# Kernel optimization log

Measured on AMD Instinct MI355X. Metric: run time of the kernel, lower is better.

## Reference

```python
import jax, jax.numpy as jnp
import numpy as np

N = 128          # preconditioner matrix dim = 8*8*2
L8 = 8           # lattice extent
KAPPA = 0.276
MAXITER = 20
NENT = N * (N + 1) // 2  # 8256 lower-triangular entries
_rows, _cols = np.tril_indices(N)

G = [jnp.array([[0, 1], [1, 0]], dtype=jnp.complex64),          # gamma_1 = sigma_x
     jnp.array([[0, -1j], [1j, 0]], dtype=jnp.complex64)]        # gamma_2 = sigma_y
I2 = jnp.eye(2, dtype=jnp.complex64)


def _D(x, U):
    # Wilson-Dirac: x (B,8,8,2) spinor field, U (B,2,8,8) complex links.
    out = x
    for mu in range(2):
        ax = mu + 1
        Um = U[:, mu]                                  # U_mu(n)
        Umb = jnp.roll(jnp.conj(Um), 1, axis=ax)       # U_mu^dag(n-mu)
        fwd = Um[..., None] * jnp.roll(x, -1, axis=ax)  # U(n) x(n+mu)
        bwd = Umb[..., None] * jnp.roll(x, 1, axis=ax)  # U^dag(n-mu) x(n-mu)
        out = out - KAPPA * (jnp.einsum('st,bxyt->bxys', I2 - G[mu], fwd)
                             + jnp.einsum('st,bxyt->bxys', I2 + G[mu], bwd))
    return out


def _Ddag(y, U):
    # Adjoint of _D: projectors swap on forward/backward hops.
    out = y
    for mu in range(2):
        ax = mu + 1
        Um = U[:, mu]
        Umb = jnp.roll(jnp.conj(Um), 1, axis=ax)
        fwd = Um[..., None] * jnp.roll(y, -1, axis=ax)
        bwd = Umb[..., None] * jnp.roll(y, 1, axis=ax)
        out = out - KAPPA * (jnp.einsum('st,bxyt->bxys', I2 + G[mu], fwd)
                             + jnp.einsum('st,bxyt->bxys', I2 - G[mu], bwd))
    return out


def setup_inputs() -> dict:
    key = jax.random.key(0)
    k1, k2, k3, k4 = jax.random.split(key, 4)
    B = 2048
    return {
        'net_out_re': jax.random.normal(k1, (B, NENT), jnp.float32),
        'net_out_im': jax.random.normal(k2, (B, NENT), jnp.float32),
        'theta': jax.random.normal(k3, (B, 2, L8, L8), jnp.float32),
        'b': jax.random.uniform(k4, (B, L8, L8, 2), jnp.float32),
    }


def reference(net_out_re, net_out_im, theta, b):
    net_out = (net_out_re + 1j * net_out_im).astype(jnp.complex64)  # (B, 8256)
    U = jnp.exp(1j * theta).astype(jnp.complex64)                   # (B, 2, 8, 8)
    bc = b.astype(jnp.complex64)                                    # (B, 8, 8, 2)
    B = bc.shape[0]

    # Dense lower-triangular factor (scatter of net_out, as in upper_tri_mat).
    Lmat = jnp.zeros((B, N, N), jnp.complex64).at[:, _rows, _cols].set(net_out)

    def M(x):  # preconditioner: L^H (L v)
        v = x.reshape(B, -1)
        w = jnp.einsum('bij,bj->bi', Lmat, v)
        u = jnp.einsum('bji,bj->bi', jnp.conj(Lmat), w)
        return u.reshape(x.shape)

    def A(x):  # DDOpt = D^dag D (Hermitian PSD)
        return _Ddag(_D(x, U), U)

    def dot(a, c):  # batched complex inner product
        return jnp.sum(jnp.conj(a) * c, axis=(1, 2, 3), keepdims=True)

    x0 = jnp.zeros_like(bc)
    r = bc - A(x0)
    z = M(r)
    p = z
    rz = dot(r, z)

    def step(carry, _):
        x, r, p, rz = carry
        Ap = A(p)
        alpha = rz / dot(p, Ap)
        x = x + alpha * p
        r = r - alpha * Ap
        z = M(r)
        rz2 = dot(r, z)
        p = z + (rz2 / rz) * p
        return (x, r, p, rz2), None

    (x, _, _, _), _ = jax.lax.scan(step, (x0, r, p, rz), None, length=MAXITER)

    res = A(x) - bc
    rn = jnp.linalg.norm(res.reshape(B, -1), axis=1)  # real per-batch norms
    return jnp.mean(rn).astype(jnp.float32)
```

## Files before the change

### kernel.cpp

```cpp
#include <hip/hip_runtime.h>
#include <math.h>

#define NV 128
#define NTRI 8256
#define NPAD8R 8960
#define KAP 0.276f
#define MAXIT 20
#define TPB 512

__device__ __forceinline__ float2 f2(float x, float y){ return make_float2(x, y); }
__device__ __forceinline__ float2 cadd(float2 a, float2 b){ return make_float2(a.x+b.x, a.y+b.y); }
__device__ __forceinline__ float2 csub(float2 a, float2 b){ return make_float2(a.x-b.x, a.y-b.y); }
__device__ __forceinline__ float2 cmul(float2 a, float2 b){ return make_float2(a.x*b.x - a.y*b.y, a.x*b.y + a.y*b.x); }
__device__ __forceinline__ float2 cmulc(float2 a, float2 b){
  return make_float2(a.x*b.x + a.y*b.y, a.x*b.y - a.y*b.x); }
__device__ __forceinline__ float2 cmac(float2 acc, float2 a, float2 b){
  acc.x = fmaf(a.x, b.x, fmaf(-a.y, b.y, acc.x));
  acc.y = fmaf(a.x, b.y, fmaf( a.y, b.x, acc.y));
  return acc; }
__device__ __forceinline__ float2 cmacc(float2 acc, float2 a, float2 b){
  acc.x = fmaf(a.x, b.x, fmaf( a.y, b.y, acc.x));
  acc.y = fmaf(a.x, b.y, fmaf(-a.y, b.x, acc.y));
  return acc; }
__device__ __forceinline__ float2 cdiv(float2 n, float2 d){
  float s = 1.0f / fmaf(d.x, d.x, d.y*d.y);
  return make_float2((n.x*d.x + n.y*d.y)*s, (n.y*d.x - n.x*d.y)*s); }

__device__ __forceinline__ int soff8(int r){
  const int a = r >> 3;
  return ((((a + 1) * ((a << 2) + (r & 7)))) << 3) + (r << 1);
}
__device__ __forceinline__ int skey(int r){ return ((r >> 1) & 3) << 1; }

__device__ __forceinline__ float2 red8(float2 v){
  v.x += __shfl_xor(v.x, 1);  v.y += __shfl_xor(v.y, 1);
  v.x += __shfl_xor(v.x, 2);  v.y += __shfl_xor(v.y, 2);
  v.x += __shfl_xor(v.x, 32); v.y += __shfl_xor(v.y, 32);
  return v;
}

template<int EF>
__device__ __forceinline__ float2 dirac_reg(const float2* __restrict__ U,
                                            const float2* __restrict__ vin, int t)
{
  const int s = t & 1, site = t >> 1;
  const int yi = site & 7, xi = site >> 3;
  const int xp = (xi+1)&7, xm = (xi-1)&7, yp = (yi+1)&7, ym = (yi-1)&7;
  float2 acc;
  {
    const int bf = (xp<<4) + (yi<<1);
    float2 fs = vin[bf + s], fo = vin[bf + (s^1)];
    float2 cf = (EF > 0) ? cadd(fs, fo) : csub(fs, fo);
    acc = cmul(U[(xi<<3)+yi], cf);
    const int bb = (xm<<4) + (yi<<1);
    float2 bs = vin[bb + s], bo = vin[bb + (s^1)];
    float2 cb = (EF > 0) ? csub(bs, bo) : cadd(bs, bo);
    acc = cadd(acc, cmulc(U[(xm<<3)+yi], cb));
  }
  {
    const float tg = s ? 1.0f : -1.0f;
    const float gf = (float)EF * tg;
    const int bf = (xi<<4) + (yp<<1);
    float2 fs = vin[bf + s], fo = vin[bf + (s^1)];
    float2 cf = make_float2(fmaf(-gf, fo.y, fs.x), fmaf(gf, fo.x, fs.y));
    acc = cadd(acc, cmul(U[64 + (xi<<3)+yi], cf));
    const float gb = -gf;
    const int bb = (xi<<4) + (ym<<1);
    float2 bs = vin[bb + s], bo = vin[bb + (s^1)];
    float2 cb = make_float2(fmaf(-gb, bo.y, bs.x), fmaf(gb, bo.x, bs.y));
    acc = cadd(acc, cmulc(U[64 + (xi<<3)+ym], cb));
  }
  float2 v0 = vin[t];
  return make_float2(fmaf(-KAP, acc.x, v0.x), fmaf(-KAP, acc.y, v0.y));
}

template<int EF>
__device__ __forceinline__ void dirac(const float2* __restrict__ U,
                                      const float2* __restrict__ vin,
                                      float2* __restrict__ vout, int t)
{
  if (t < NV) vout[t] = dirac_reg<EF>(U, vin, t);
  __syncthreads();
}

__device__ __forceinline__ void precond(const float2* __restrict__ Lc2,
                                        const float2* __restrict__ vin,
                                        float2* __restrict__ wvv,
                                        float2* __restrict__ vout,
                                        float2* __restrict__ scal,
                                        int w, int lane)
{
  const int c  = lane & 3;
  const int g  = lane >> 2;
  const int q  = g & 7;
  const int h  = g >> 3;
  const int c2 = c << 1;
  const int rlo = (w << 3) + q;
  const int rhi = 127 - rlo;
  const int bLo = soff8(rlo);
  const int bHi = soff8(rhi);
  const int keyLo = skey(rlo);
  const int keyHi = skey(rhi);

  {
    float2 a0 = f2(0.f, 0.f), a1 = f2(0.f, 0.f);
    #pragma unroll
    for (int i = 0; i < 8; ++i) {
      if (i <= w) {
        const int k    = h ? (8 - w + i) : i;
        const int base = h ? bHi : bLo;
        const int keyR = h ? keyHi : keyLo;
        const float4 Lp = *(const float4*)&Lc2[base + (k << 3) + c2];
        const float4 vp = *(const float4*)&vin[(k << 3) + (c2 ^ keyR)];
        a0 = cmac(cmac(a0, f2(Lp.x,Lp.y), f2(vp.x,vp.y)), f2(Lp.z,Lp.w), f2(vp.z,vp.w));
      } else {
        const int k  = h ? (8 - w + i) : (i - w - 1);
        const float4 Lp = *(const float4*)&Lc2[bHi + (k << 3) + c2];
        const float4 vp = *(const float4*)&vin[(k << 3) + (c2 ^ keyHi)];
        a1 = cmac(cmac(a1, f2(Lp.x,Lp.y), f2(vp.x,vp.y)), f2(Lp.z,Lp.w), f2(vp.z,vp.w));
      }
    }
    if (!h) {
      const int k = 7 - w;
      const float4 Lp = *(const float4*)&Lc2[bHi + (k << 3) + c2];
      const float4 vp = *(const float4*)&vin[(k << 3) + (c2 ^ keyHi)];
      a1 = cmac(cmac(a1, f2(Lp.x,Lp.y), f2(vp.x,vp.y)), f2(Lp.z,Lp.w), f2(vp.z,vp.w));
    }
    float2 vLo = h ? f2(0.f, 0.f) : a0;
    float2 vHi = h ? cadd(a0, a1) : a1;
    vLo = red8(vLo);
    vHi = red8(vHi);
    if (c == 0) wvv[h ? rhi : rlo] = h ? vHi : vLo;
  }
  __syncthreads();

  {
    const int key2 = c2;
    float2 a0 = f2(0.f, 0.f), a1 = f2(0.f, 0.f);
    #pragma unroll
    for (int i = 0; i < 8; ++i) {
      int k, j;
      if (i <= w) {
        k = h ? (8 + i) : (15 - w + i);
        j = h ? rlo : rhi;
      } else {
        k = h ? (8 + i) : (i - 1);
        j = rlo;
      }
      const int u    = (k + 1) << 3;
      const int off0 = u * ((k << 2) + c2) + (k << 4) + (c2 << 1) + (j ^ key2);
      const int off1 = off0 + u + 2;
      const int i0   = (k << 3) + c2;
      const float2 La = Lc2[off0];
      const float2 Lb = Lc2[off1];
      const float4 wp = *(const float4*)&wvv[i0];
      if (i <= w) a0 = cmacc(cmacc(a0, La, f2(wp.x,wp.y)), Lb, f2(wp.z,wp.w));
      else        a1 = cmacc(cmacc(a1, La, f2(wp.x,wp.y)), Lb, f2(wp.z,wp.w));
    }
    if (!h) {
      const int o0 = (64 * (28 + c2)) + 112 + (c2 << 1) + (rlo ^ key2);
      const float2 La = Lc2[o0];
      const float2 Lb = Lc2[o0 + 66];
      const float4 wp = *(const float4*)&wvv[56 + c2];
      a1 = cmacc(cmacc(a1, La, f2(wp.x,wp.y)), Lb, f2(wp.z,wp.w));
    }
    float2 vJhi = h ? f2(0.f, 0.f) : a0;
    float2 vJlo = h ? cadd(a0, a1) : a1;
    vJhi = red8(vJhi);
    vJlo = red8(vJlo);
    float2 dotp = f2(0.f, 0.f);
    if (c == 0) {
      const int jw = h ? rlo : rhi;
      const float2 zj = h ? vJlo : vJhi;
      vout[jw] = zj;
      dotp = cmacc(f2(0.f, 0.f), vin[jw], zj);
    }
    #pragma unroll
    for (int off = 32; off >= 4; off >>= 1) {
      dotp.x += __shfl_down(dotp.x, off, 64);
      dotp.y += __shfl_down(dotp.y, off, 64);
    }
    if (lane == 0) scal[w] = dotp;
  }
  __syncthreads();
}

extern "C" __global__ void __launch_bounds__(TPB, 4)
cg_loss_kernel(const float* __restrict__ nre, const float* __restrict__ nim,
               const float* __restrict__ theta, const float* __restrict__ bin,
               float* __restrict__ out, float invB)
{
  __shared__ __align__(16) float2 Lc2[NPAD8R];
  __shared__ __align__(16) float2 Uc[128];
  __shared__ __align__(16) float2 bv[NV], rv[NV], pv[NV];
  __shared__ __align__(16) float2 zv[NV], tv[NV], wv[NV];
  __shared__ float2 scal[12];

  const int t = threadIdx.x;
  const long long b = blockIdx.x;
  const int w = t >> 6, lane = t & 63;

  for (int p = t; p < NPAD8R; p += TPB) Lc2[p] = make_float2(0.f, 0.f);
  float2 xr = f2(0.f, 0.f), rr = f2(0.f, 0.f), pr = f2(0.f, 0.f), rz = f2(1.f, 0.f);
  if (t < NV) {
    float th = theta[b * 128 + t];
    float sn, cs;
    sincosf(th, &sn, &cs);
    Uc[t] = make_float2(cs, sn);
    float bb = bin[b * 128 + t];
    bv[t] = make_float2(bb, 0.f);
    rr = make_float2(bb, 0.f);
    rv[t] = rr;
  }
  __syncthreads();

  {
    const float* nreb = nre + b * NTRI;
    const float* nimb = nim + b * NTRI;
    for (int p = t; p < NTRI; p += TPB) {
      float re = nreb[p], im = nimb[p];
      int r = (int)((sqrtf(8.f * (float)p + 1.f) - 1.f) * 0.5f + 1e-3f);
      int tr = (r * (r + 1)) >> 1;
      if (tr > p)               { tr -= r; --r; }
      else if (tr + r + 1 <= p) { tr += r + 1; ++r; }
      Lc2[soff8(r) + ((p - tr) ^ skey(r))] = make_float2(re, im);
    }
  }
  __syncthreads();

  precond(Lc2, rv, wv, zv, scal, w, lane);
  if (t < NV) {
    rz = cadd(cadd(cadd(scal[0],scal[1]), cadd(scal[2],scal[3])),
              cadd(cadd(scal[4],scal[5]), cadd(scal[6],scal[7])));
    pr = zv[t];
    pv[t] = pr;
  }
  __syncthreads();

  #pragma unroll 1
  for (int it = 0; it < MAXIT - 1; ++it) {
    dirac<-1>(Uc, pv, tv, t);
    float2 ap = f2(0.f, 0.f);
    if (t < NV) {
      ap = dirac_reg<+1>(Uc, tv, t);
      float2 v = cmacc(f2(0.f,0.f), pr, ap);
      #pragma unroll
      for (int off = 32; off > 0; off >>= 1) {
        v.x += __shfl_down(v.x, off, 64);
        v.y += __shfl_down(v.y, off, 64);
      }
      if ((t & 63) == 0) scal[8 + (t >> 6)] = v;
    }
    __syncthreads();
    if (t < NV) {
      float2 alpha = cdiv(rz, cadd(scal[8], scal[9]));
      xr = cmac(xr, alpha, pr);
      rr = csub(rr, cmul(alpha, ap));
      rv[t] = rr;
    }
    __syncthreads();
    precond(Lc2, rv, wv, zv, scal, w, lane);
    if (t < NV) {
      float2 rz2 = cadd(cadd(cadd(scal[0],scal[1]), cadd(scal[2],scal[3])),
                        cadd(cadd(scal[4],scal[5]), cadd(scal[6],scal[7])));
      float2 beta = cdiv(rz2, rz);
      rz = rz2;
      pr = cmac(zv[t], beta, pr);
      pv[t] = pr;
    }
    __syncthreads();
  }

  dirac<-1>(Uc, pv, tv, t);
  {
    float2 ap = f2(0.f, 0.f);
    if (t < NV) {
      ap = dirac_reg<+1>(Uc, tv, t);
      float2 v = cmacc(f2(0.f,0.f), pr, ap);
      #pragma unroll
      for (int off = 32; off > 0; off >>= 1) {
        v.x += __shfl_down(v.x, off, 64);
        v.y += __shfl_down(v.y, off, 64);
      }
      if ((t & 63) == 0) scal[8 + (t >> 6)] = v;
    }
    __syncthreads();
    if (t < NV) {
      float2 alpha = cdiv(rz, cadd(scal[8], scal[9]));
      xr = cmac(xr, alpha, pr);
      rv[t] = xr;
    }
    __syncthreads();
  }

  dirac<-1>(Uc, rv, tv, t);
  if (t < NV) {
    float2 ax = dirac_reg<+1>(Uc, tv, t);
    float2 d = csub(ax, bv[t]);
    float v = fmaf(d.x, d.x, d.y * d.y);
    #pragma unroll
    for (int off = 32; off > 0; off >>= 1) v += __shfl_down(v, off, 64);
    if ((t & 63) == 0) scal[10 + (t >> 6)].x = v;
  }
  __syncthreads();
  if (t == 0) {
    float rn = sqrtf(scal[10].x + scal[11].x);
    atomicAdd(out, rn * invB);
  }
}

extern "C" void kernel_launch(void* const* d_in, const int* in_sizes, int n_in,
                              void* d_out, int out_size, void* d_ws, size_t ws_size,
                              hipStream_t stream)
{
  const float* nre   = (const float*)d_in[0];
  const float* nim   = (const float*)d_in[1];
  const float* theta = (const float*)d_in[2];
  const float* bin   = (const float*)d_in[3];
  float* out = (float*)d_out;
  const int B = in_sizes[0] / NTRI;

  hipMemsetAsync(out, 0, sizeof(float), stream);
  cg_loss_kernel<<<B, TPB, 0, stream>>>(nre, nim, theta, bin, out, 1.0f / (float)B);
}
```

Baseline: 514.8 us.

## Spread preconditioner matvec over 16 waves with 1024-thread blocks

Doubles threads per block and remaps the triangular L and L^H matvecs so each wave handles 4 row pairs split into 4 segment groups, reducing per-lane serial work. Reductions are widened to 16 lanes and the partial dots are summed across 16 waves. The shared b buffer is removed and b is reread from global memory for the final residual. The risk is more barrier cost and more idle threads during the 128-thread Dirac and CG phases.

```diff
diff --git a/kernel.cpp b/kernel.cpp
--- a/kernel.cpp
+++ b/kernel.cpp
@@ -6,7 +6,7 @@
 #define NPAD8R 8960
 #define KAP 0.276f
 #define MAXIT 20
-#define TPB 512
+#define TPB 1024
 
 __device__ __forceinline__ float2 f2(float x, float y){ return make_float2(x, y); }
 __device__ __forceinline__ float2 cadd(float2 a, float2 b){ return make_float2(a.x+b.x, a.y+b.y); }
@@ -32,9 +32,10 @@
 }
 __device__ __forceinline__ int skey(int r){ return ((r >> 1) & 3) << 1; }
 
-__device__ __forceinline__ float2 red8(float2 v){
+__device__ __forceinline__ float2 red16(float2 v){
   v.x += __shfl_xor(v.x, 1);  v.y += __shfl_xor(v.y, 1);
   v.x += __shfl_xor(v.x, 2);  v.y += __shfl_xor(v.y, 2);
+  v.x += __shfl_xor(v.x, 16); v.y += __shfl_xor(v.y, 16);
   v.x += __shfl_xor(v.x, 32); v.y += __shfl_xor(v.y, 32);
   return v;
 }
@@ -83,118 +84,104 @@
   __syncthreads();
 }
 
-__device__ __forceinline__ void precond(const float2* __restrict__ Lc2,
-                                        const float2* __restrict__ vin,
-                                        float2* __restrict__ wvv,
-                                        float2* __restrict__ vout,
-                                        float2* __restrict__ scal,
-                                        int w, int lane)
+__device__ __forceinline__ void precond16(const float2* __restrict__ Lc2,
+                                          const float2* __restrict__ vin,
+                                          float2* __restrict__ wvv,
+                                          float2* __restrict__ vout,
+                                          float2* __restrict__ scal,
+                                          int w, int lane)
 {
   const int c  = lane & 3;
-  const int g  = lane >> 2;
-  const int q  = g & 7;
-  const int h  = g >> 3;
+  const int pq = (lane >> 2) & 3;
+  const int s  = lane >> 4;
   const int c2 = c << 1;
-  const int rlo = (w << 3) + q;
+  const int rlo = (w << 2) + pq;
   const int rhi = 127 - rlo;
-  const int bLo = soff8(rlo);
-  const int bHi = soff8(rhi);
-  const int keyLo = skey(rlo);
-  const int keyHi = skey(rhi);
-
-  {
-    float2 a0 = f2(0.f, 0.f), a1 = f2(0.f, 0.f);
+  const int w2  = rlo >> 3;
+  const int nlo = w2 + 1;
+  const int bLo = soff8(rlo), bHi = soff8(rhi);
+  const int keyLo = skey(rlo), keyHi = skey(rhi);
+
+  {
+    float2 a0 = f2(0.f,0.f), a1 = f2(0.f,0.f);
     #pragma unroll
-    for (int i = 0; i < 8; ++i) {
-      if (i <= w) {
-        const int k    = h ? (8 - w + i) : i;
-        const int base = h ? bHi : bLo;
-        const int keyR = h ? keyHi : keyLo;
-        const float4 Lp = *(const float4*)&Lc2[base + (k << 3) + c2];
-        const float4 vp = *(const float4*)&vin[(k << 3) + (c2 ^ keyR)];
-        a0 = cmac(cmac(a0, f2(Lp.x,Lp.y), f2(vp.x,vp.y)), f2(Lp.z,Lp.w), f2(vp.z,vp.w));
-      } else {
-        const int k  = h ? (8 - w + i) : (i - w - 1);
-        const float4 Lp = *(const float4*)&Lc2[bHi + (k << 3) + c2];
-        const float4 vp = *(const float4*)&vin[(k << 3) + (c2 ^ keyHi)];
-        a1 = cmac(cmac(a1, f2(Lp.x,Lp.y), f2(vp.x,vp.y)), f2(Lp.z,Lp.w), f2(vp.z,vp.w));
-      }
-    }
-    if (!h) {
-      const int k = 7 - w;
+    for (int ii = 0; ii < 4; ++ii) {
+      const int e    = (ii << 2) + s;
+      const bool lo  = (e < nlo);
+      const int k    = lo ? e : (e - nlo);
+      const int base = lo ? bLo : bHi;
+      const int key  = lo ? keyLo : keyHi;
+      const float4 Lp = *(const float4*)&Lc2[base + (k << 3) + c2];
+      const float4 vp = *(const float4*)&vin[(k << 3) + (c2 ^ key)];
+      if (lo) a0 = cmac(cmac(a0, f2(Lp.x,Lp.y), f2(vp.x,vp.y)), f2(Lp.z,Lp.w), f2(vp.z,vp.w));
+      else    a1 = cmac(cmac(a1, f2(Lp.x,Lp.y), f2(vp.x,vp.y)), f2(Lp.z,Lp.w), f2(vp.z,vp.w));
+    }
+    if (s == 0) {
+      const int k = 16 - nlo;
       const float4 Lp = *(const float4*)&Lc2[bHi + (k << 3) + c2];
       const float4 vp = *(const float4*)&vin[(k << 3) + (c2 ^ keyHi)];
       a1 = cmac(cmac(a1, f2(Lp.x,Lp.y), f2(vp.x,vp.y)), f2(Lp.z,Lp.w), f2(vp.z,vp.w));
     }
-    float2 vLo = h ? f2(0.f, 0.f) : a0;
-    float2 vHi = h ? cadd(a0, a1) : a1;
-    vLo = red8(vLo);
-    vHi = red8(vHi);
-    if (c == 0) wvv[h ? rhi : rlo] = h ? vHi : vLo;
-  }
-  __syncthreads();
-
-  {
-    const int key2 = c2;
-    float2 a0 = f2(0.f, 0.f), a1 = f2(0.f, 0.f);
+    float2 vLo = red16(a0);
+    float2 vHi = red16(a1);
+    if (c == 0 && s == 0) wvv[rlo] = vLo;
+    if (c == 0 && s == 1) wvv[rhi] = vHi;
+  }
+  __syncthreads();
+
+  {
+    float2 a0 = f2(0.f,0.f), a1 = f2(0.f,0.f);
     #pragma unroll
-    for (int i = 0; i < 8; ++i) {
-      int k, j;
-      if (i <= w) {
-        k = h ? (8 + i) : (15 - w + i);
-        j = h ? rlo : rhi;
-      } else {
-        k = h ? (8 + i) : (i - 1);
-        j = rlo;
-      }
+    for (int ii = 0; ii < 4; ++ii) {
+      const int e   = (ii << 2) + s;
+      const bool hi = (e < nlo);
+      const int k = hi ? (15 - w2 + e) : (e - 1);
+      const int j = hi ? rhi : rlo;
       const int u    = (k + 1) << 3;
-      const int off0 = u * ((k << 2) + c2) + (k << 4) + (c2 << 1) + (j ^ key2);
-      const int off1 = off0 + u + 2;
-      const int i0   = (k << 3) + c2;
+      const int off0 = u * ((k << 2) + c2) + (k << 4) + (c2 << 1) + (j ^ c2);
       const float2 La = Lc2[off0];
-      const float2 Lb = Lc2[off1];
-      const float4 wp = *(const float4*)&wvv[i0];
-      if (i <= w) a0 = cmacc(cmacc(a0, La, f2(wp.x,wp.y)), Lb, f2(wp.z,wp.w));
-      else        a1 = cmacc(cmacc(a1, La, f2(wp.x,wp.y)), Lb, f2(wp.z,wp.w));
-    }
-    if (!h) {
-      const int o0 = (64 * (28 + c2)) + 112 + (c2 << 1) + (rlo ^ key2);
-      const float2 La = Lc2[o0];
-      const float2 Lb = Lc2[o0 + 66];
-      const float4 wp = *(const float4*)&wvv[56 + c2];
+      const float2 Lb = Lc2[off0 + u + 2];
+      const float4 wp = *(const float4*)&wvv[(k << 3) + c2];
+      if (hi) a0 = cmacc(cmacc(a0, La, f2(wp.x,wp.y)), Lb, f2(wp.z,wp.w));
+      else    a1 = cmacc(cmacc(a1, La, f2(wp.x,wp.y)), Lb, f2(wp.z,wp.w));
+    }
+    if (s == 0) {
+      const int off0 = 128 * (60 + c2) + 240 + (c2 << 1) + (rlo ^ c2);
+      const float2 La = Lc2[off0];
+      const float2 Lb = Lc2[off0 + 130];
+      const float4 wp = *(const float4*)&wvv[120 + c2];
       a1 = cmacc(cmacc(a1, La, f2(wp.x,wp.y)), Lb, f2(wp.z,wp.w));
     }
-    float2 vJhi = h ? f2(0.f, 0.f) : a0;
-    float2 vJlo = h ? cadd(a0, a1) : a1;
-    vJhi = red8(vJhi);
-    vJlo = red8(vJlo);
-    float2 dotp = f2(0.f, 0.f);
-    if (c == 0) {
-      const int jw = h ? rlo : rhi;
-      const float2 zj = h ? vJlo : vJhi;
-      vout[jw] = zj;
-      dotp = cmacc(f2(0.f, 0.f), vin[jw], zj);
-    }
-    #pragma unroll
-    for (int off = 32; off >= 4; off >>= 1) {
-      dotp.x += __shfl_down(dotp.x, off, 64);
-      dotp.y += __shfl_down(dotp.y, off, 64);
-    }
+    float2 vJhi = red16(a0);
+    float2 vJlo = red16(a1);
+    float2 dotp = f2(0.f,0.f);
+    if (c == 0 && s == 0) { vout[rhi] = vJhi; dotp = cmacc(f2(0.f,0.f), vin[rhi], vJhi); }
+    if (c == 0 && s == 1) { vout[rlo] = vJlo; dotp = cmacc(f2(0.f,0.f), vin[rlo], vJlo); }
+    dotp.x += __shfl_xor(dotp.x, 4);  dotp.y += __shfl_xor(dotp.y, 4);
+    dotp.x += __shfl_xor(dotp.x, 8);  dotp.y += __shfl_xor(dotp.y, 8);
+    dotp.x += __shfl_xor(dotp.x, 16); dotp.y += __shfl_xor(dotp.y, 16);
     if (lane == 0) scal[w] = dotp;
   }
   __syncthreads();
 }
 
-extern "C" __global__ void __launch_bounds__(TPB, 4)
+__device__ __forceinline__ float2 sum16(const float2* __restrict__ scal)
+{
+  float2 r = scal[0];
+  #pragma unroll
+  for (int i = 1; i < 16; ++i) r = cadd(r, scal[i]);
+  return r;
+}
+
+extern "C" __global__ void __launch_bounds__(TPB, 8)
 cg_loss_kernel(const float* __restrict__ nre, const float* __restrict__ nim,
                const float* __restrict__ theta, const float* __restrict__ bin,
                float* __restrict__ out, float invB)
 {
   __shared__ __align__(16) float2 Lc2[NPAD8R];
   __shared__ __align__(16) float2 Uc[128];
-  __shared__ __align__(16) float2 bv[NV], rv[NV], pv[NV];
-  __shared__ __align__(16) float2 zv[NV], tv[NV], wv[NV];
-  __shared__ float2 scal[12];
+  __shared__ __align__(16) float2 rv[NV], pv[NV], tv[NV], wv[NV], zv[NV];
+  __shared__ float2 scal[20];
 
   const int t = threadIdx.x;
   const long long b = blockIdx.x;
@@ -208,7 +195,6 @@
     sincosf(th, &sn, &cs);
     Uc[t] = make_float2(cs, sn);
     float bb = bin[b * 128 + t];
-    bv[t] = make_float2(bb, 0.f);
     rr = make_float2(bb, 0.f);
     rv[t] = rr;
   }
@@ -228,10 +214,9 @@
   }
   __syncthreads();
 
-  precond(Lc2, rv, wv, zv, scal, w, lane);
+  precond16(Lc2, rv, wv, zv, scal, w, lane);
   if (t < NV) {
-    rz = cadd(cadd(cadd(scal[0],scal[1]), cadd(scal[2],scal[3])),
-              cadd(cadd(scal[4],scal[5]), cadd(scal[6],scal[7])));
+    rz = sum16(scal);
     pr = zv[t];
     pv[t] = pr;
   }
@@ -249,20 +234,19 @@
         v.x += __shfl_down(v.x, off, 64);
         v.y += __shfl_down(v.y, off, 64);
       }
-      if ((t & 63) == 0) scal[8 + (t >> 6)] = v;
-    }
-    __syncthreads();
-    if (t < NV) {
-      float2 alpha = cdiv(rz, cadd(scal[8], scal[9]));
+      if ((t & 63) == 0) scal[16 + (t >> 6)] = v;
+    }
+    __syncthreads();
+    if (t < NV) {
+      float2 alpha = cdiv(rz, cadd(scal[16], scal[17]));
       xr = cmac(xr, alpha, pr);
       rr = csub(rr, cmul(alpha, ap));
       rv[t] = rr;
     }
     __syncthreads();
-    precond(Lc2, rv, wv, zv, scal, w, lane);
-    if (t < NV) {
-      float2 rz2 = cadd(cadd(cadd(scal[0],scal[1]), cadd(scal[2],scal[3])),
-                        cadd(cadd(scal[4],scal[5]), cadd(scal[6],scal[7])));
+    precond16(Lc2, rv, wv, zv, scal, w, lane);
+    if (t < NV) {
+      float2 rz2 = sum16(scal);
       float2 beta = cdiv(rz2, rz);
       rz = rz2;
       pr = cmac(zv[t], beta, pr);
@@ -282,11 +266,11 @@
         v.x += __shfl_down(v.x, off, 64);
         v.y += __shfl_down(v.y, off, 64);
       }
-      if ((t & 63) == 0) scal[8 + (t >> 6)] = v;
-    }
-    __syncthreads();
-    if (t < NV) {
-      float2 alpha = cdiv(rz, cadd(scal[8], scal[9]));
+      if ((t & 63) == 0) scal[16 + (t >> 6)] = v;
+    }
+    __syncthreads();
+    if (t < NV) {
+      float2 alpha = cdiv(rz, cadd(scal[16], scal[17]));
       xr = cmac(xr, alpha, pr);
       rv[t] = xr;
     }
@@ -296,15 +280,16 @@
   dirac<-1>(Uc, rv, tv, t);
   if (t < NV) {
     float2 ax = dirac_reg<+1>(Uc, tv, t);
-    float2 d = csub(ax, bv[t]);
-    float v = fmaf(d.x, d.x, d.y * d.y);
+    float bb = bin[b * 128 + t];
+    float dx = ax.x - bb, dy = ax.y;
+    float v = fmaf(dx, dx, dy * dy);
     #pragma unroll
     for (int off = 32; off > 0; off >>= 1) v += __shfl_down(v, off, 64);
-    if ((t & 63) == 0) scal[10 + (t >> 6)].x = v;
+    if ((t & 63) == 0) scal[18 + (t >> 6)].x = v;
   }
   __syncthreads();
   if (t == 0) {
-    float rn = sqrtf(scal[10].x + scal[11].x);
+    float rn = sqrtf(scal[18].x + scal[19].x);
     atomicAdd(out, rn * invB);
   }
 }
```

Result: slower. 0.9998 ms (+94.2%).
